# Kernel tuning notes

Measured on AMD Instinct MI355X. Metric: run time of the kernel, lower is better.

Reference implementation:

```python
import jax, jax.numpy as jnp
import numpy as np

B, C, H, W = 64, 128, 56, 56
ALPHA = 0.001


def _build_inhi_mat(out_channels):
    # Circulant 0/1 band: row i has ones at columns (i-r//2 ... i+r//2) mod C,
    # exactly matching the torch double loop with modular wrap-around.
    r = out_channels // 8 + 1  # inhiRange
    i = np.arange(out_channels)[:, None]
    d = np.arange(-(r // 2), r // 2 + 1)[None, :]
    cols = (i + d) % out_channels  # [C, r]
    m = np.zeros((out_channels, out_channels), dtype=np.float32)
    m[np.repeat(i, d.shape[1], axis=1), cols] = 1.0
    return m


def setup_inputs() -> dict:
    key = jax.random.key(0)
    x = jax.random.normal(key, (B, C, H, W), dtype=jnp.float32)
    inhiMat = jnp.asarray(_build_inhi_mat(C))  # [C, C] constant buffer
    return {"x": x, "inhiMat": inhiMat}


def reference(x, inhiMat):
    b, c, h, w = x.shape
    inhiRange = c // 8 + 1
    # y = detach(x)^2 -> banded cross-channel sum (bmm with broadcast [C,C] mat)
    y = jax.lax.stop_gradient(x) ** 2
    y = y.reshape(b, c, h * w)
    y = jnp.einsum('ij,bjs->bis', inhiMat, y)  # same math as bmm with tiled inhi
    y = y.reshape(b, c, h, w)
    denom = (y * ALPHA / inhiRange + 1.0) ** 0.75
    return x / denom
```

## Files before the change

kernel.cpp:

```cpp
#include <hip/hip_runtime.h>


#define HW4 784
#define CSTR HW4
#define BSTR4 (128 * HW4)
#define NCOL4 (64 * HW4)
#define TILE 16
#define SEGC 32
#define PLANES 48
#define NBLK (NCOL4 / TILE)

typedef __attribute__((address_space(3))) unsigned int lds_u32;
typedef __attribute__((address_space(1))) const unsigned int glb_u32;

__device__ __forceinline__ float pow_m075(float t) {
    return __builtin_amdgcn_exp2f(-0.75f * __builtin_amdgcn_logf(t));
}

__global__ __launch_bounds__(256) void lrn_kernel(const float4* __restrict__ x,
                                                  float4* __restrict__ out) {
    const float kAlphaOverR = 0.001f / 17.0f;

    __shared__ float4 lds[4 * PLANES * TILE];

    const int tid  = threadIdx.x;
    const int lane = tid & 63;
    const int wave = tid >> 6;
    const int band = wave * SEGC;

    float4* buf = &lds[wave * (PLANES * TILE)];

    const int cl    = lane & 15;
    const int g     = lane >> 4;
    const int col4g = blockIdx.x * TILE + cl;
    const int b     = col4g / HW4;
    const int hw4   = col4g - b * HW4;
    const float4* xbase = x + (size_t)b * BSTR4 + hw4;
    float4*       obase = out + (size_t)b * BSTR4 + hw4;

#pragma unroll
    for (int q = 0; q < 12; ++q) {
        const int ch = (band - 8 + 4 * q + g + 128) & 127;
        __builtin_amdgcn_global_load_lds((glb_u32*)(xbase + (size_t)ch * CSTR),
                                         (lds_u32*)&buf[q * 64], 16, 0, 0);
    }
    asm volatile("s_waitcnt vmcnt(0)" ::: "memory");

    float sx = 0.f, sy = 0.f, sz = 0.f, sw = 0.f;
#pragma unroll
    for (int j = 0; j < 17; ++j) {
        const float4 v = buf[(g * 8 + j) * TILE + cl];
        sx = fmaf(v.x, v.x, sx);
        sy = fmaf(v.y, v.y, sy);
        sz = fmaf(v.z, v.z, sz);
        sw = fmaf(v.w, v.w, sw);
    }

#pragma unroll
    for (int i = 0; i < 8; ++i) {
        const int j = g * 8 + 8 + i;
        const float4 xc = buf[j * TILE + cl];
        float4 o;
        o.x = xc.x * pow_m075(fmaf(sx, kAlphaOverR, 1.0f));
        o.y = xc.y * pow_m075(fmaf(sy, kAlphaOverR, 1.0f));
        o.z = xc.z * pow_m075(fmaf(sz, kAlphaOverR, 1.0f));
        o.w = xc.w * pow_m075(fmaf(sw, kAlphaOverR, 1.0f));
        obase[(size_t)(band + g * 8 + i) * CSTR] = o;

        if (i < 7) {
            const float4 a = buf[(j + 9) * TILE + cl];
            const float4 d = buf[(j - 8) * TILE + cl];
            sx += a.x * a.x - d.x * d.x;
            sy += a.y * a.y - d.y * d.y;
            sz += a.z * a.z - d.z * d.z;
            sw += a.w * a.w - d.w * d.w;
        }
    }
}

extern "C" void kernel_launch(void* const* d_in, const int* in_sizes, int n_in,
                              void* d_out, int out_size, void* d_ws, size_t ws_size,
                              hipStream_t stream) {
    const float4* x = (const float4*)d_in[0];
    float4* out = (float4*)d_out;

    dim3 grid(NBLK);
    lrn_kernel<<<grid, 256, 0, stream>>>(x, out);
}
```

Before: 182.3 us.

## Use producer wave streaming channels into LDS ring with barrier-synced consumer waves

Replaces the per-tile independent loads with a warp-specialized pipeline. One wave streams channel planes (half an image plane each) into a 24-slot LDS ring via async global-to-LDS loads, and seven consumer waves walk 64 channels with a running window sum, synchronized per step by barriers. It aims to raise the reuse of loaded planes and keep many loads in flight. The cost is one block per CU, only 256 blocks, and barrier overhead on every channel step. Block count and occupancy drop a lot, which may leave HBM bandwidth underused.

New measurement: 187.7 us. +2.9%, slower.

```diff
diff --git a/kernel.cpp b/kernel.cpp
--- a/kernel.cpp
+++ b/kernel.cpp
@@ -1,14 +1,11 @@
 #include <hip/hip_runtime.h>
 
 
-#define HW4 784
-#define CSTR HW4
-#define BSTR4 (128 * HW4)
-#define NCOL4 (64 * HW4)
-#define TILE 16
-#define SEGC 32
-#define PLANES 48
-#define NBLK (NCOL4 / TILE)
+#define HW4   784
+#define HALF4 392
+#define RING  24
+#define NSTEP 64
+#define NCHNK 80
 
 typedef __attribute__((address_space(3))) unsigned int lds_u32;
 typedef __attribute__((address_space(1))) const unsigned int glb_u32;
@@ -17,63 +14,97 @@
     return __builtin_amdgcn_exp2f(-0.75f * __builtin_amdgcn_logf(t));
 }
 
-__global__ __launch_bounds__(256) void lrn_kernel(const float4* __restrict__ x,
-                                                  float4* __restrict__ out) {
+__global__ __launch_bounds__(512, 1) void lrn_kernel(const float4* __restrict__ x,
+                                                     float4* __restrict__ out) {
     const float kAlphaOverR = 0.001f / 17.0f;
 
-    __shared__ float4 lds[4 * PLANES * TILE];
+    __shared__ float4 ring[RING * HALF4];
 
     const int tid  = threadIdx.x;
-    const int lane = tid & 63;
     const int wave = tid >> 6;
-    const int band = wave * SEGC;
 
-    float4* buf = &lds[wave * (PLANES * TILE)];
+    const int blk  = blockIdx.x;
+    const int b    = blk >> 2;
+    const int h    = (blk >> 1) & 1;
+    const int band = (blk & 1) << 6;
 
-    const int cl    = lane & 15;
-    const int g     = lane >> 4;
-    const int col4g = blockIdx.x * TILE + cl;
-    const int b     = col4g / HW4;
-    const int hw4   = col4g - b * HW4;
-    const float4* xbase = x + (size_t)b * BSTR4 + hw4;
-    float4*       obase = out + (size_t)b * BSTR4 + hw4;
+    if (wave == 0) {
+        const int lane = tid & 63;
+        const float4* pb = x + ((size_t)b * 128) * HW4 + h * HALF4 + lane;
+        int chp  = (band + 120) & 127;
+        int slot = 0;
 
-#pragma unroll
-    for (int q = 0; q < 12; ++q) {
-        const int ch = (band - 8 + 4 * q + g + 128) & 127;
-        __builtin_amdgcn_global_load_lds((glb_u32*)(xbase + (size_t)ch * CSTR),
-                                         (lds_u32*)&buf[q * 64], 16, 0, 0);
-    }
-    asm volatile("s_waitcnt vmcnt(0)" ::: "memory");
+        auto issue = [&]() {
+            const float4* s = pb + (size_t)chp * HW4;
+            float4* d = &ring[slot * HALF4];
+            __builtin_amdgcn_global_load_lds((glb_u32*)(s +   0), (lds_u32*)(d +   0), 16, 0, 0);
+            __builtin_amdgcn_global_load_lds((glb_u32*)(s +  64), (lds_u32*)(d +  64), 16, 0, 0);
+            __builtin_amdgcn_global_load_lds((glb_u32*)(s + 128), (lds_u32*)(d + 128), 16, 0, 0);
+            __builtin_amdgcn_global_load_lds((glb_u32*)(s + 192), (lds_u32*)(d + 192), 16, 0, 0);
+            __builtin_amdgcn_global_load_lds((glb_u32*)(s + 256), (lds_u32*)(d + 256), 16, 0, 0);
+            __builtin_amdgcn_global_load_lds((glb_u32*)(s + 320), (lds_u32*)(d + 320), 16, 0, 0);
+            __builtin_amdgcn_global_load_lds((glb_u32*)(s + 328), (lds_u32*)(d + 328), 16, 0, 0);
+            chp = (chp + 1) & 127;
+            slot = (slot + 1 == RING) ? 0 : slot + 1;
+        };
 
-    float sx = 0.f, sy = 0.f, sz = 0.f, sw = 0.f;
-#pragma unroll
-    for (int j = 0; j < 17; ++j) {
-        const float4 v = buf[(g * 8 + j) * TILE + cl];
-        sx = fmaf(v.x, v.x, sx);
-        sy = fmaf(v.y, v.y, sy);
-        sz = fmaf(v.z, v.z, sz);
-        sw = fmaf(v.w, v.w, sw);
-    }
+        for (int p = 0; p < 22; ++p) issue();
+        asm volatile("s_waitcnt vmcnt(35)" ::: "memory");
+        __builtin_amdgcn_s_barrier();
 
-#pragma unroll
-    for (int i = 0; i < 8; ++i) {
-        const int j = g * 8 + 8 + i;
-        const float4 xc = buf[j * TILE + cl];
-        float4 o;
-        o.x = xc.x * pow_m075(fmaf(sx, kAlphaOverR, 1.0f));
-        o.y = xc.y * pow_m075(fmaf(sy, kAlphaOverR, 1.0f));
-        o.z = xc.z * pow_m075(fmaf(sz, kAlphaOverR, 1.0f));
-        o.w = xc.w * pow_m075(fmaf(sw, kAlphaOverR, 1.0f));
-        obase[(size_t)(band + g * 8 + i) * CSTR] = o;
+        for (int j = 0; j < 58; ++j) {
+            issue();
+            asm volatile("s_waitcnt vmcnt(35)" ::: "memory");
+            __builtin_amdgcn_s_barrier();
+        }
+        asm volatile("s_waitcnt vmcnt(28)" ::: "memory"); __builtin_amdgcn_s_barrier();
+        asm volatile("s_waitcnt vmcnt(21)" ::: "memory"); __builtin_amdgcn_s_barrier();
+        asm volatile("s_waitcnt vmcnt(14)" ::: "memory"); __builtin_amdgcn_s_barrier();
+        asm volatile("s_waitcnt vmcnt(7)"  ::: "memory"); __builtin_amdgcn_s_barrier();
+        asm volatile("s_waitcnt vmcnt(0)"  ::: "memory"); __builtin_amdgcn_s_barrier();
+        __builtin_amdgcn_s_barrier();
+    } else {
+        const int  ctid = tid - 64;
+        const bool act  = ctid < HALF4;
+        float4* op = out + ((size_t)(b * 128 + band)) * HW4 + h * HALF4 + ctid;
 
-        if (i < 7) {
-            const float4 a = buf[(j + 9) * TILE + cl];
-            const float4 d = buf[(j - 8) * TILE + cl];
-            sx += a.x * a.x - d.x * d.x;
-            sy += a.y * a.y - d.y * d.y;
-            sz += a.z * a.z - d.z * d.z;
-            sw += a.w * a.w - d.w * d.w;
+        __builtin_amdgcn_s_barrier();
+
+        float sx = 0.f, sy = 0.f, sz = 0.f, sw = 0.f;
+        if (act) {
+            for (int p = 0; p < 17; ++p) {
+                const float4 v = ring[p * HALF4 + ctid];
+                sx = fmaf(v.x, v.x, sx);
+                sy = fmaf(v.y, v.y, sy);
+                sz = fmaf(v.z, v.z, sz);
+                sw = fmaf(v.w, v.w, sw);
+            }
+        }
+
+        int ia = 16, id = 23, ix = 8;
+        for (int j = 0; j < NSTEP; ++j) {
+            if (act) {
+                if (j > 0) {
+                    const float4 a = ring[ia * HALF4 + ctid];
+                    const float4 d = ring[id * HALF4 + ctid];
+                    sx += a.x * a.x - d.x * d.x;
+                    sy += a.y * a.y - d.y * d.y;
+                    sz += a.z * a.z - d.z * d.z;
+                    sw += a.w * a.w - d.w * d.w;
+                }
+                const float4 xc = ring[ix * HALF4 + ctid];
+                float4 o;
+                o.x = xc.x * pow_m075(fmaf(sx, kAlphaOverR, 1.0f));
+                o.y = xc.y * pow_m075(fmaf(sy, kAlphaOverR, 1.0f));
+                o.z = xc.z * pow_m075(fmaf(sz, kAlphaOverR, 1.0f));
+                o.w = xc.w * pow_m075(fmaf(sw, kAlphaOverR, 1.0f));
+                *op = o;
+                op += HW4;
+            }
+            ia = (ia + 1 == RING) ? 0 : ia + 1;
+            id = (id + 1 == RING) ? 0 : id + 1;
+            ix = (ix + 1 == RING) ? 0 : ix + 1;
+            __builtin_amdgcn_s_barrier();
         }
     }
 }
@@ -84,6 +115,6 @@
     const float4* x = (const float4*)d_in[0];
     float4* out = (float4*)d_out;
 
-    dim3 grid(NBLK);
-    lrn_kernel<<<grid, 256, 0, stream>>>(x, out);
+    dim3 grid(64 * 2 * 2);
+    lrn_kernel<<<grid, 512, 0, stream>>>(x, out);
 }
```
